# Kernel tuning notes

Hardware: AMD Instinct MI355X
Metric: run time of the kernel (lower is better)

The kernel has to match this reference:

```python
import jax, jax.numpy as jnp
import numpy as np
from jax import lax

K = 3      # kernel_size
STRIDE = 1
PAD = 1
N_BASIS = 8


def _cheb_basis(x, n):
    # Chebyshev basis T_k(tanh(x)), k = 1..n  -> (..., n)
    t = jnp.arccos(jnp.tanh(x))
    ks = jnp.arange(1, n + 1, dtype=x.dtype)
    return jnp.cos(t[..., None] * ks)


def setup_inputs() -> dict:
    key = jax.random.key(0)
    k1, k2, k3 = jax.random.split(key, 3)
    b, cin, h, w = 16, 16, 64, 64
    cout = 32
    x = jax.random.normal(k1, (b, cin, h, w), dtype=jnp.float32)
    # params as in __init__: normal_(w), normal_(c, 0, 0.001)
    w_p = jax.random.normal(k2, (cin, cout, K * K, 1), dtype=jnp.float32)
    c_p = jax.random.normal(k3, (cin, cout, K * K, 1, N_BASIS), dtype=jnp.float32) * 0.001
    return {"x": x, "w": w_p, "c": c_p}


def reference(x, w, c):
    b, cin, h, wd = x.shape
    ho = (h - K + 2 * PAD) // STRIDE + 1
    wo = (wd - K + 2 * PAD) // STRIDE + 1
    L = ho * wo
    # unfold: (b, cin*K*K, ho, wo), channel-major like F.unfold
    patches = lax.conv_general_dilated_patches(
        x, (K, K), (STRIDE, STRIDE), [(PAD, PAD), (PAD, PAD)])
    wx = patches.reshape(b, cin, K * K, L)            # (b,i,k,l)
    res = jax.nn.silu(wx)                              # residual activation
    basis = _cheb_basis(wx, N_BASIS)                   # (b,i,k,l,n)
    w_sq = w[..., 0]                                   # (i,o,k)
    c_sq = c[:, :, :, 0, :]                            # (i,o,k,n)
    # sum_{i,k} w[i,o,k] * (res[b,i,k,l] + sum_n c[i,o,k,n]*basis[b,i,k,l,n])
    out = (jnp.einsum('iok,bikl->bol', w_sq, res)
           + jnp.einsum('iokn,bikln->bol', w_sq[..., None] * c_sq, basis))
    return out.reshape(b, -1, ho, wo)
```

## Files before the change

kernel.cpp:

```cpp
#include <hip/hip_runtime.h>

#define CIN 16
#define COUT 32
#define NB 8
#define HW 4096
#define PPW 66
#define KF 160
#define NCH 20
#define FROWS 6
#define PLANE 397

typedef short bf16x8 __attribute__((ext_vector_type(8)));
typedef float f32x16 __attribute__((ext_vector_type(16)));

__device__ inline unsigned short f2bf(float f) {
    unsigned u = __builtin_bit_cast(unsigned, f);
    u += 0x7FFFu + ((u >> 16) & 1u);
    return (unsigned short)(u >> 16);
}
__device__ inline unsigned pk(float a, float b) {
    return (unsigned)f2bf(a) | ((unsigned)f2bf(b) << 16);
}

#define FEAT_SHORTS (NCH * PLANE * 8)
#define LDS_BYTES (FEAT_SHORTS * 2 + 8 * 1024 * 4)

__global__ __launch_bounds__(512) void kan_wf(const float* __restrict__ w,
                                              const float* __restrict__ c,
                                              unsigned short* __restrict__ wfl) {
    const int t = blockIdx.x * 512 + threadIdx.x;
    const int e    = t & 7;
    const int lane = (t >> 3) & 63;
    const int frag = t >> 9;
    const int shift = frag / 10;
    const int st    = frag % 10;
    const int o     = lane & 31;
    const int kel   = st * 16 + (lane >> 5) * 8 + e;
    const int i     = kel / 10, n = kel % 10;
    float val = 0.f;
    if (n != 9) {
        const float wv = w[(size_t)(i * COUT + o) * 9 + shift];
        val = (n == 0) ? wv : wv * c[((size_t)(i * COUT + o) * 9 + shift) * NB + (n - 1)];
    }
    wfl[t] = f2bf(val);
}

__global__ __launch_bounds__(1024, 4) void kan_main(const float* __restrict__ x,
                                                    const unsigned short* __restrict__ wfl,
                                                    float* __restrict__ out) {
    extern __shared__ __align__(16) unsigned short lds[];

    const int bid = blockIdx.x;
    const int b   = bid >> 4;
    const int y0  = (bid & 15) * 4;
    const int tid = threadIdx.x;

    for (int item = tid; item < 4 * FROWS * PPW; item += 1024) {
        const int cg  = item / (FROWS * PPW);
        const int rem = item - cg * (FROWS * PPW);
        const int lr  = rem / PPW;
        const int px  = rem - lr * PPW;
        const int iy  = y0 + lr - 1;

        unsigned rw[20];
        const bool valid = (iy >= 0) & (iy < 64) & (px >= 1) & (px <= 64);
        if (valid) {
            const int ix = px - 1;
#pragma unroll
            for (int j = 0; j < 4; ++j) {
                const int i = cg * 4 + j;
                const float v  = x[((size_t)(b * CIN + i)) * HW + iy * 64 + ix];
                const float p  = __expf(-v);
                const float p2 = p * p;
                const float s  = v * __builtin_amdgcn_rcpf(1.f + p);
                const float u  = (1.f - p2) * __builtin_amdgcn_rcpf(1.f + p2);
                const float u2 = 2.f * u;
                const float t1 = u;
                const float t2 = u2 * u - 1.f;
                const float t3 = u2 * t2 - t1;
                const float t4 = u2 * t3 - t2;
                const float t5 = u2 * t4 - t3;
                const float t6 = u2 * t5 - t4;
                const float t7 = u2 * t6 - t5;
                const float t8 = u2 * t7 - t6;
                rw[j * 5 + 0] = pk(s, t1);
                rw[j * 5 + 1] = pk(t2, t3);
                rw[j * 5 + 2] = pk(t4, t5);
                rw[j * 5 + 3] = pk(t6, t7);
                rw[j * 5 + 4] = (unsigned)f2bf(t8);
            }
        } else {
#pragma unroll
            for (int j = 0; j < 20; ++j) rw[j] = 0u;
        }
        const int base = lr * PPW + px;
#pragma unroll
        for (int q = 0; q < 5; ++q)
            *(uint4*)&lds[((cg * 5 + q) * PLANE + base) * 8] =
                make_uint4(rw[4 * q], rw[4 * q + 1], rw[4 * q + 2], rw[4 * q + 3]);
    }

    __syncthreads();

    const int l    = tid & 63;
    const int wv   = tid >> 6;
    const int pg   = wv >> 1;
    const int par  = wv & 1;
    const int ry   = pg >> 1;
    const int x0   = (pg & 1) * 32;
    const int colp = l & 31;
    const int hi   = l >> 5;

    const unsigned short* abase = wfl + l * 8;

    f32x16 acc;
#pragma unroll
    for (int r = 0; r < 16; ++r) acc[r] = 0.f;

#pragma unroll
    for (int shift = 0; shift < 9; ++shift) {
        const int dy = shift / 3 - 1, dx = shift % 3 - 1;
        const int base = (ry + 1 + dy) * PPW + (x0 + colp + 1 + dx);
        const unsigned short* aq = abase + (shift * 10 + par) * 512;
        const unsigned short* bb = lds + ((2 * par + hi) * PLANE + base) * 8;
#pragma unroll
        for (int t = 0; t < 5; ++t) {
            const bf16x8 bf = *(const bf16x8*)(bb + (size_t)(4 * t) * PLANE * 8);
            const bf16x8 av = *(const bf16x8*)(aq + (2 * t) * 512);
            acc = __builtin_amdgcn_mfma_f32_32x32x16_bf16(av, bf, acc, 0, 0, 0);
        }
    }

    float* red = (float*)(lds + FEAT_SHORTS);
    if (par) {
#pragma unroll
        for (int r = 0; r < 16; ++r) red[pg * 1024 + r * 64 + l] = acc[r];
    }
    __syncthreads();
    if (!par) {
        float* op = out + (size_t)b * COUT * HW + (y0 + ry) * 64 + x0 + colp;
#pragma unroll
        for (int r = 0; r < 16; ++r) {
            const float v = acc[r] + red[pg * 1024 + r * 64 + l];
            const int o = (r & 3) + 8 * (r >> 2) + 4 * hi;
            op[(size_t)o * HW] = v;
        }
    }
}

extern "C" void kernel_launch(void* const* d_in, const int* in_sizes, int n_in,
                              void* d_out, int out_size, void* d_ws, size_t ws_size,
                              hipStream_t stream) {
    const float* x = (const float*)d_in[0];
    const float* w = (const float*)d_in[1];
    const float* c = (const float*)d_in[2];
    float* out = (float*)d_out;

    unsigned short* wfl = (unsigned short*)d_ws;

    hipFuncSetAttribute((const void*)kan_main,
                        hipFuncAttributeMaxDynamicSharedMemorySize, LDS_BYTES);

    kan_wf<<<90, 512, 0, stream>>>(w, c, wfl);
    kan_main<<<256, 1024, LDS_BYTES, stream>>>(x, wfl, out);
}
```

Baseline: 21.29 us.

## Reuse A fragments across two column tiles and split K four ways per row

Each wave now covers a full 64-pixel row as two 32-column MFMA tiles that share one weight-fragment load, and K-steps are split across four waves instead of two. The reduction buffer now reuses the feature LDS region after an extra barrier, which shrinks the dynamic LDS allocation. The intent is to halve global A-fragment loads per MFMA and cut LDS footprint. The trade-off is uneven K work (3/3/2/2 steps per wave), a larger three-way cross-wave reduction, and twice the accumulator registers.

Result: slower. 23.80 us (+11.8%).

```diff
diff --git a/kernel.cpp b/kernel.cpp
--- a/kernel.cpp
+++ b/kernel.cpp
@@ -23,7 +23,7 @@
 }
 
 #define FEAT_SHORTS (NCH * PLANE * 8)
-#define LDS_BYTES (FEAT_SHORTS * 2 + 8 * 1024 * 4)
+#define LDS_BYTES (FEAT_SHORTS * 2)
 
 __global__ __launch_bounds__(512) void kan_wf(const float* __restrict__ w,
                                               const float* __restrict__ c,
@@ -104,46 +104,59 @@
 
     const int l    = tid & 63;
     const int wv   = tid >> 6;
-    const int pg   = wv >> 1;
-    const int par  = wv & 1;
-    const int ry   = pg >> 1;
-    const int x0   = (pg & 1) * 32;
+    const int pg   = wv >> 2;
+    const int par  = wv & 3;
     const int colp = l & 31;
     const int hi   = l >> 5;
 
     const unsigned short* abase = wfl + l * 8;
 
-    f32x16 acc;
+    f32x16 acc0, acc1;
 #pragma unroll
-    for (int r = 0; r < 16; ++r) acc[r] = 0.f;
+    for (int r = 0; r < 16; ++r) { acc0[r] = 0.f; acc1[r] = 0.f; }
 
 #pragma unroll
     for (int shift = 0; shift < 9; ++shift) {
         const int dy = shift / 3 - 1, dx = shift % 3 - 1;
-        const int base = (ry + 1 + dy) * PPW + (x0 + colp + 1 + dx);
-        const unsigned short* aq = abase + (shift * 10 + par) * 512;
-        const unsigned short* bb = lds + ((2 * par + hi) * PLANE + base) * 8;
+        const int rbase = (pg + 1 + dy) * PPW + (colp + 1 + dx);
 #pragma unroll
-        for (int t = 0; t < 5; ++t) {
-            const bf16x8 bf = *(const bf16x8*)(bb + (size_t)(4 * t) * PLANE * 8);
-            const bf16x8 av = *(const bf16x8*)(aq + (2 * t) * 512);
-            acc = __builtin_amdgcn_mfma_f32_32x32x16_bf16(av, bf, acc, 0, 0, 0);
+        for (int t = 0; t < 3; ++t) {
+            const int st = par + 4 * t;
+            if (st >= 10) break;
+            const bf16x8 av = *(const bf16x8*)(abase + (shift * 10 + st) * 512);
+            const unsigned short* bb = lds + ((st * 2 + hi) * PLANE + rbase) * 8;
+            const bf16x8 bf0 = *(const bf16x8*)(bb);
+            const bf16x8 bf1 = *(const bf16x8*)(bb + 32 * 8);
+            acc0 = __builtin_amdgcn_mfma_f32_32x32x16_bf16(av, bf0, acc0, 0, 0, 0);
+            acc1 = __builtin_amdgcn_mfma_f32_32x32x16_bf16(av, bf1, acc1, 0, 0, 0);
         }
     }
 
-    float* red = (float*)(lds + FEAT_SHORTS);
+    __syncthreads();
+    float* red = (float*)lds;
     if (par) {
+        const int base = (((par - 1) * 4 + pg) * 2) * 1024;
 #pragma unroll
-        for (int r = 0; r < 16; ++r) red[pg * 1024 + r * 64 + l] = acc[r];
+        for (int r = 0; r < 16; ++r) {
+            red[base + r * 64 + l]        = acc0[r];
+            red[base + 1024 + r * 64 + l] = acc1[r];
+        }
     }
     __syncthreads();
-    if (!par) {
-        float* op = out + (size_t)b * COUT * HW + (y0 + ry) * 64 + x0 + colp;
+    if (par == 0) {
+        float* op = out + (size_t)b * COUT * HW + (y0 + pg) * 64 + colp;
 #pragma unroll
         for (int r = 0; r < 16; ++r) {
-            const float v = acc[r] + red[pg * 1024 + r * 64 + l];
+            float v0 = acc0[r], v1 = acc1[r];
+#pragma unroll
+            for (int p = 1; p < 4; ++p) {
+                const int base = (((p - 1) * 4 + pg) * 2) * 1024;
+                v0 += red[base + r * 64 + l];
+                v1 += red[base + 1024 + r * 64 + l];
+            }
             const int o = (r & 3) + 8 * (r >> 2) + 4 * hi;
-            op[(size_t)o * HW] = v;
+            op[(size_t)o * HW]      = v0;
+            op[(size_t)o * HW + 32] = v1;
         }
     }
 }
```
